# Performance work log

Hardware: AMD Instinct MI355X
Metric: run time of the kernel (lower is better)

Reference implementation:

```python
import jax, jax.numpy as jnp
import numpy as np

D_MODEL = 1024
NUM_HEADS = 16
HEAD_DIM = D_MODEL // NUM_HEADS


def setup_inputs() -> dict:
    key = jax.random.key(0)
    ks = jax.random.split(key, 11)
    B, S = 2, 2048
    s = 1.0 / np.sqrt(D_MODEL)
    return {
        "q": jax.random.normal(ks[0], (B, S, D_MODEL), jnp.float32),
        "k": jax.random.normal(ks[1], (B, S, D_MODEL), jnp.float32),
        "v": jax.random.normal(ks[2], (B, S, D_MODEL), jnp.float32),
        "Wq": jax.random.normal(ks[3], (D_MODEL, D_MODEL), jnp.float32) * s,
        "bq": jnp.zeros((D_MODEL,), jnp.float32),
        "Wk": jax.random.normal(ks[4], (D_MODEL, D_MODEL), jnp.float32) * s,
        "bk": jnp.zeros((D_MODEL,), jnp.float32),
        "Wv": jax.random.normal(ks[5], (D_MODEL, D_MODEL), jnp.float32) * s,
        "bv": jnp.zeros((D_MODEL,), jnp.float32),
        "Wo": jax.random.normal(ks[6], (D_MODEL, D_MODEL), jnp.float32) * s,
        "bo": jnp.zeros((D_MODEL,), jnp.float32),
    }


def _split_heads(x):
    B, S, _ = x.shape
    return x.reshape(B, S, NUM_HEADS, HEAD_DIM).transpose(0, 2, 1, 3)  # [B,H,S,Dh]


def reference(q, k, v, Wq, bq, Wk, bk, Wv, bv, Wo, bo):
    B, S, _ = q.shape
    qh = _split_heads(q @ Wq.T + bq)
    kh = _split_heads(k @ Wk.T + bk)
    vh = _split_heads(v @ Wv.T + bv)
    scale = 1.0 / jnp.sqrt(jnp.asarray(HEAD_DIM, qh.dtype))
    scores = jnp.einsum("bhqd,bhkd->bhqk", qh, kh) * scale  # [B,H,S,S]
    attn = jax.nn.softmax(scores, axis=-1)
    out = jnp.einsum("bhqk,bhkd->bhqd", attn, vh)
    out = out.transpose(0, 2, 1, 3).reshape(B, S, D_MODEL)
    return out @ Wo.T + bo
```

## Files before the change

kernel.cpp:

```cpp
#include <hip/hip_runtime.h>
#include <cstdint>
#include <cstddef>

#define DEVI __device__ __forceinline__

typedef short bf16x8 __attribute__((ext_vector_type(8)));
typedef short bf16x4 __attribute__((ext_vector_type(4)));
typedef float f32x4 __attribute__((ext_vector_type(4)));
typedef float f32x16 __attribute__((ext_vector_type(16)));
typedef unsigned short u16x4 __attribute__((ext_vector_type(4)));

constexpr int D_MODEL = 1024;
constexpr int HEADS = 16;
constexpr int DH = 64;
constexpr int SEQ = 2048;
constexpr int KDIM = 1024;

DEVI unsigned short f2bf(float f) {
  union { float f; unsigned u; } v; v.f = f;
  unsigned r = v.u + 0x7fffu + ((v.u >> 16) & 1u);
  return (unsigned short)(r >> 16);
}

DEVI unsigned pkbf(float a, float b) {
  return __builtin_amdgcn_perm(__float_as_uint(b), __float_as_uint(a), 0x07060302u);
}

DEVI void cp16(const void* g, void* l) {
  __builtin_amdgcn_global_load_lds(
      (const __attribute__((address_space(1))) void*)g,
      (__attribute__((address_space(3))) void*)l, 16, 0, 0);
}

DEVI f32x16 mfma_32x32x8(bf16x4 a, bf16x4 b, f32x16 c) {
#if __has_builtin(__builtin_amdgcn_mfma_f32_32x32x8bf16_1k)
  return __builtin_amdgcn_mfma_f32_32x32x8bf16_1k(a, b, c, 0, 0, 0);
#else
  asm volatile("v_mfma_f32_32x32x8_bf16 %0, %1, %2, %0" : "+v"(c) : "v"(a), "v"(b));
  return c;
#endif
}

#define BAR()        asm volatile("s_barrier" ::: "memory")
#define WAITVM(n)    asm volatile("s_waitcnt vmcnt(" #n ")" ::: "memory")

__global__ void __launch_bounds__(256) castall(
    const float* __restrict__ q, const float* __restrict__ k, const float* __restrict__ v,
    const float* __restrict__ Wq, const float* __restrict__ Wk,
    const float* __restrict__ Wv, const float* __restrict__ Wo,
    unsigned short* __restrict__ qb, unsigned short* __restrict__ kb, unsigned short* __restrict__ vb,
    unsigned short* __restrict__ Wqb, unsigned short* __restrict__ Wkb,
    unsigned short* __restrict__ Wvb, unsigned short* __restrict__ Wob) {
  int bid = blockIdx.x;
  const float* s; unsigned short* d; int off;
  if (bid < 12288) {
    int w = bid >> 12; off = bid & 4095;
    s = (w == 0) ? q : ((w == 1) ? k : v);
    d = (w == 0) ? qb : ((w == 1) ? kb : vb);
  } else {
    int w = (bid - 12288) >> 10; off = bid & 1023;
    s = (w == 0) ? Wq : ((w == 1) ? Wk : ((w == 2) ? Wv : Wo));
    d = (w == 0) ? Wqb : ((w == 1) ? Wkb : ((w == 2) ? Wvb : Wob));
  }
  int i = (off * 256 + threadIdx.x) * 4;
  float4 x = *(const float4*)(s + i);
  u16x4 o; o[0] = f2bf(x.x); o[1] = f2bf(x.y); o[2] = f2bf(x.z); o[3] = f2bf(x.w);
  *(u16x4*)(d + i) = o;
}

__global__ void __launch_bounds__(256) qkv_gemm(
    const unsigned short* __restrict__ qb, const unsigned short* __restrict__ kb,
    const unsigned short* __restrict__ vb,
    const unsigned short* __restrict__ Wqb, const unsigned short* __restrict__ Wkb,
    const unsigned short* __restrict__ Wvb,
    const float* __restrict__ bq, const float* __restrict__ bk, const float* __restrict__ bv,
    unsigned short* __restrict__ Qh, unsigned short* __restrict__ Kh,
    unsigned short* __restrict__ Vt, float qscale) {
  __shared__ unsigned short As[3][128 * 32];
  __shared__ unsigned short Bs[3][128 * 32];
  const int bid = blockIdx.x, seg = bid >> 8, inner = bid & 255;
  const int bm = inner & 31, bn = inner >> 5;
  const unsigned short* A = (seg == 0) ? qb : ((seg == 1) ? kb : vb);
  const unsigned short* W = (seg == 0) ? Wqb : ((seg == 1) ? Wkb : Wvb);
  const float* bias = (seg == 0) ? bq : ((seg == 1) ? bk : bv);
  unsigned short* O = (seg == 0) ? Qh : ((seg == 1) ? Kh : Vt);
  const float oscale = (seg == 0) ? qscale : 1.0f;
  const int mode = (seg == 2) ? 1 : 0;

  const int tid = threadIdx.x, lane = tid & 63, wave = tid >> 6;
  const int l16 = lane & 15, quad = lane >> 4;
  const int wm = (wave >> 1) * 64, wn = (wave & 1) * 64;
  const int sw = (l16 >> 1) & 3;
  f32x4 acc[4][4] = {};

  const int r0 = tid >> 2, p0 = tid & 3;
  const int c0 = (p0 ^ ((r0 >> 1) & 3)) * 8;
  const int r1 = (256 + tid) >> 2;
  const int c1 = (p0 ^ ((r1 >> 1) & 3)) * 8;
  const unsigned short* Arow0 = A + (size_t)(bm * 128 + r0) * KDIM + c0;
  const unsigned short* Arow1 = A + (size_t)(bm * 128 + r1) * KDIM + c1;
  const unsigned short* Wrow0 = W + (size_t)(bn * 128 + r0) * KDIM + c0;
  const unsigned short* Wrow1 = W + (size_t)(bn * 128 + r1) * KDIM + c1;

#define QKV_ISSUE(K0, P)                                    \
  do {                                                      \
    cp16(Arow0 + (K0), &As[P][tid * 8]);                    \
    cp16(Arow1 + (K0), &As[P][(256 + tid) * 8]);            \
    cp16(Wrow0 + (K0), &Bs[P][tid * 8]);                    \
    cp16(Wrow1 + (K0), &Bs[P][(256 + tid) * 8]);            \
  } while (0)

#define QKV_COMPUTE(P)                                                             \
  do {                                                                             \
    bf16x8 af[4], bfr[4];                                                          \
    _Pragma("unroll") for (int t = 0; t < 4; ++t)                                  \
        af[t] = *(const bf16x8*)&As[P][(wm + t * 16 + l16) * 32 + ((quad ^ sw) * 8)]; \
    _Pragma("unroll") for (int t = 0; t < 4; ++t)                                  \
        bfr[t] = *(const bf16x8*)&Bs[P][(wn + t * 16 + l16) * 32 + ((quad ^ sw) * 8)]; \
    _Pragma("unroll") for (int i = 0; i < 4; ++i)                                  \
        _Pragma("unroll") for (int j = 0; j < 4; ++j)                              \
            acc[i][j] = __builtin_amdgcn_mfma_f32_16x16x32_bf16(af[i], bfr[j],     \
                                                                acc[i][j], 0, 0, 0); \
  } while (0)

  QKV_ISSUE(0, 0);
  QKV_ISSUE(32, 1);
  for (int k = 0; k < 30; k += 3) {
    BAR(); QKV_ISSUE((k + 2) * 32, 2); WAITVM(8); BAR(); QKV_COMPUTE(0);
    BAR(); QKV_ISSUE((k + 3) * 32, 0); WAITVM(8); BAR(); QKV_COMPUTE(1);
    BAR(); QKV_ISSUE((k + 4) * 32, 1); WAITVM(8); BAR(); QKV_COMPUTE(2);
  }
  WAITVM(4); BAR(); QKV_COMPUTE(0);
  WAITVM(0); BAR(); QKV_COMPUTE(1);

#pragma unroll
  for (int i = 0; i < 4; ++i) {
#pragma unroll
    for (int j = 0; j < 4; ++j) {
      const int col = bn * 128 + wn + j * 16 + l16;
      const float bv = bias[col];
#pragma unroll
      for (int r = 0; r < 4; ++r) {
        const int row = bm * 128 + wm + i * 16 + quad * 4 + r;
        const float val = (acc[i][j][r] + bv) * oscale;
        const int b = row >> 11, s = row & (SEQ - 1);
        const int h = col >> 6, d = col & (DH - 1);
        size_t idx;
        if (mode == 0) idx = ((size_t)(b * HEADS + h) * SEQ + s) * DH + d;
        else           idx = ((size_t)(b * HEADS + h) * DH + d) * SEQ + s;
        O[idx] = f2bf(val);
      }
    }
  }
#undef QKV_ISSUE
#undef QKV_COMPUTE
}

__global__ void __launch_bounds__(256) out_gemm(const unsigned short* __restrict__ AO,
                                                const unsigned short* __restrict__ Wob,
                                                const float* __restrict__ bo,
                                                float* __restrict__ out) {
  __shared__ unsigned short As[3][64 * 32];
  __shared__ unsigned short Bs[3][128 * 32];
  const int bid = blockIdx.x, bm = bid & 63, bn = bid >> 6;
  const int tid = threadIdx.x, lane = tid & 63, wave = tid >> 6;
  const int l16 = lane & 15, quad = lane >> 4;
  const int wn = wave * 32;
  const int sw = (l16 >> 1) & 3;
  f32x4 acc[4][2] = {};

  const int ra = tid >> 2, pa = tid & 3;
  const int ca = (pa ^ ((ra >> 1) & 3)) * 8;
  const int r1 = (256 + tid) >> 2;
  const int c1 = (pa ^ ((r1 >> 1) & 3)) * 8;
  const unsigned short* Arow  = AO + (size_t)(bm * 64 + ra) * KDIM + ca;
  const unsigned short* Wrow0 = Wob + (size_t)(bn * 128 + ra) * KDIM + ca;
  const unsigned short* Wrow1 = Wob + (size_t)(bn * 128 + r1) * KDIM + c1;

#define OUT_ISSUE(K0, P)                                    \
  do {                                                      \
    cp16(Arow + (K0), &As[P][tid * 8]);                     \
    cp16(Wrow0 + (K0), &Bs[P][tid * 8]);                    \
    cp16(Wrow1 + (K0), &Bs[P][(256 + tid) * 8]);            \
  } while (0)

#define OUT_COMPUTE(P)                                                             \
  do {                                                                             \
    bf16x8 af[4], bfr[2];                                                          \
    _Pragma("unroll") for (int t = 0; t < 4; ++t)                                  \
        af[t] = *(const bf16x8*)&As[P][(t * 16 + l16) * 32 + ((quad ^ sw) * 8)];   \
    _Pragma("unroll") for (int u = 0; u < 2; ++u)                                  \
        bfr[u] = *(const bf16x8*)&Bs[P][(wn + u * 16 + l16) * 32 + ((quad ^ sw) * 8)]; \
    _Pragma("unroll") for (int i = 0; i < 4; ++i)                                  \
        _Pragma("unroll") for (int j = 0; j < 2; ++j)                              \
            acc[i][j] = __builtin_amdgcn_mfma_f32_16x16x32_bf16(af[i], bfr[j],     \
                                                                acc[i][j], 0, 0, 0); \
  } while (0)

  OUT_ISSUE(0, 0);
  OUT_ISSUE(32, 1);
  for (int k = 0; k < 30; k += 3) {
    BAR(); OUT_ISSUE((k + 2) * 32, 2); WAITVM(6); BAR(); OUT_COMPUTE(0);
    BAR(); OUT_ISSUE((k + 3) * 32, 0); WAITVM(6); BAR(); OUT_COMPUTE(1);
    BAR(); OUT_ISSUE((k + 4) * 32, 1); WAITVM(6); BAR(); OUT_COMPUTE(2);
  }
  WAITVM(3); BAR(); OUT_COMPUTE(0);
  WAITVM(0); BAR(); OUT_COMPUTE(1);

#pragma unroll
  for (int i = 0; i < 4; ++i)
#pragma unroll
    for (int j = 0; j < 2; ++j) {
      const int col = bn * 128 + wn + j * 16 + l16;
      const float bv = bo[col];
#pragma unroll
      for (int r = 0; r < 4; ++r) {
        const int row = bm * 64 + i * 16 + quad * 4 + r;
        out[(size_t)row * D_MODEL + col] = acc[i][j][r] + bv;
      }
    }
#undef OUT_ISSUE
#undef OUT_COMPUTE
}

__global__ void __launch_bounds__(256) attn(const unsigned short* __restrict__ Qh,
                                            const unsigned short* __restrict__ Kh,
                                            const unsigned short* __restrict__ Vt,
                                            unsigned short* __restrict__ AO) {
  __shared__ __align__(16) char smem[32768];
  unsigned short* Ks = (unsigned short*)smem;
  unsigned short* Vs = (unsigned short*)(smem + 16384);

  const int bid = blockIdx.x;
  const int qt = bid >> 5, head = bid & 31, b = head >> 4, h = head & 15;
  const int tid = threadIdx.x;
  const int lane = tid & 63, wave = tid >> 6;
  const int wq = wave >> 1, wk = wave & 1;
  const int l31 = lane & 31, hh = lane >> 5;

  const unsigned short* Qhead = Qh + (size_t)(b * HEADS + h) * SEQ * DH;
  const unsigned short* Khead = Kh + (size_t)(b * HEADS + h) * SEQ * DH;
  const unsigned short* Vhead = Vt + (size_t)(b * HEADS + h) * DH * SEQ;

  const int qrow = qt * 64 + wq * 32 + l31;
  bf16x8 aq[4];
#pragma unroll
  for (int it = 0; it < 4; ++it)
    aq[it] = *(const bf16x8*)&Qhead[(size_t)qrow * DH + it * 16 + hh * 8];

  f32x16 oacc[2] = {};
  float lsum = 0.f;

  for (int kc = 0; kc < SEQ / 128; ++kc) {
#pragma unroll
    for (int c = 0; c < 4; ++c) {
      int s = c * 256 + tid;
      int row = s >> 3, pblk = s & 7;
      int jb = pblk ^ (row & 7);
      cp16(Khead + (size_t)(kc * 128 + row) * DH + jb * 8, &Ks[s * 8]);
    }
#pragma unroll
    for (int c = 0; c < 4; ++c) {
      int s = c * 256 + tid;
      int d = s >> 4, pblk = s & 15;
      int jb = pblk ^ (d & 7);
      cp16(Vhead + (size_t)d * SEQ + kc * 128 + jb * 8, &Vs[s * 8]);
    }
    asm volatile("s_waitcnt vmcnt(0)" ::: "memory");
    __syncthreads();

#pragma unroll
    for (int sub = 0; sub < 2; ++sub) {
      const int kb32 = sub * 64 + wk * 32;
      const int key = kb32 + l31;

      f32x16 sa = {};
#pragma unroll
      for (int it = 0; it < 4; ++it) {
        const int sblk = (2 * it + hh) ^ (key & 7);
        bf16x8 ak = *(const bf16x8*)&Ks[key * 64 + sblk * 8];
        sa = __builtin_amdgcn_mfma_f32_32x32x16_bf16(ak, aq[it], sa, 0, 0, 0);
      }

      float p[16];
#pragma unroll
      for (int r = 0; r < 16; ++r) {
        p[r] = __builtin_amdgcn_exp2f(sa[r]);
        lsum += p[r];
      }
      bf16x4 pk[4];
#pragma unroll
      for (int g = 0; g < 4; ++g) {
        union { unsigned u[2]; bf16x4 s; } c;
        c.u[0] = pkbf(p[4 * g + 0], p[4 * g + 1]);
        c.u[1] = pkbf(p[4 * g + 2], p[4 * g + 3]);
        pk[g] = c.s;
      }

#pragma unroll
      for (int g = 0; g < 4; ++g) {
        const int gblk = sub * 8 + wk * 4 + g;
#pragma unroll
        for (int dh2 = 0; dh2 < 2; ++dh2) {
          const int d = dh2 * 32 + l31;
          const int sv = gblk ^ (d & 7);
          bf16x4 av = *(const bf16x4*)&Vs[d * 128 + sv * 8 + hh * 4];
          oacc[dh2] = mfma_32x32x8(av, pk[g], oacc[dh2]);
        }
      }
    }
    __syncthreads();
  }

  lsum += __shfl_xor(lsum, 32);

  float* epiF = (float*)smem;
  float* lbuf = (float*)(smem + 16384);
  unsigned short* Oq = (unsigned short*)(smem + 17408);

  if (l31 == lane) lbuf[wave * 32 + l31] = lsum;
  if (wk == 1) {
#pragma unroll
    for (int dh2 = 0; dh2 < 2; ++dh2)
#pragma unroll
      for (int r = 0; r < 16; ++r) {
        const int d = dh2 * 32 + (r & 3) + 8 * (r >> 2) + 4 * hh;
        epiF[wq * 2048 + d * 32 + l31] = oacc[dh2][r];
      }
  }
  __syncthreads();

  if (wk == 0) {
    const float linv = 1.0f / (lsum + lbuf[(wq * 2 + 1) * 32 + l31]);
#pragma unroll
    for (int dh2 = 0; dh2 < 2; ++dh2) {
#pragma unroll
      for (int r = 0; r < 16; r += 2) {
        const int d = dh2 * 32 + (r & 3) + 8 * (r >> 2) + 4 * hh;
        const float v0 = (oacc[dh2][r]     + epiF[wq * 2048 + d * 32 + l31]) * linv;
        const float v1 = (oacc[dh2][r + 1] + epiF[wq * 2048 + (d + 1) * 32 + l31]) * linv;
        *(unsigned*)&Oq[wq * 2176 + l31 * 68 + d] = pkbf(v0, v1);
      }
    }
  }
  __syncthreads();

  {
    const int qloc = tid >> 2, d0 = (tid & 3) * 16;
    const int base = (qloc >> 5) * 2176 + (qloc & 31) * 68 + d0;
    unsigned u[8];
#pragma unroll
    for (int i = 0; i < 8; ++i) u[i] = *(const unsigned*)&Oq[base + i * 2];
    unsigned short* dst = AO + ((size_t)(b * SEQ + qt * 64 + qloc)) * D_MODEL + h * 64 + d0;
    *(uint4*)dst       = make_uint4(u[0], u[1], u[2], u[3]);
    *(uint4*)(dst + 8) = make_uint4(u[4], u[5], u[6], u[7]);
  }
}

extern "C" void kernel_launch(void* const* d_in, const int* in_sizes, int n_in,
                              void* d_out, int out_size, void* d_ws, size_t ws_size,
                              hipStream_t stream) {
  const float* q  = (const float*)d_in[0];
  const float* k  = (const float*)d_in[1];
  const float* v  = (const float*)d_in[2];
  const float* Wq = (const float*)d_in[3];
  const float* bq = (const float*)d_in[4];
  const float* Wk = (const float*)d_in[5];
  const float* bk = (const float*)d_in[6];
  const float* Wv = (const float*)d_in[7];
  const float* bv = (const float*)d_in[8];
  const float* Wo = (const float*)d_in[9];
  const float* bo = (const float*)d_in[10];
  float* out = (float*)d_out;

  char* ws = (char*)d_ws;
  const size_t MB = 1ull << 20;
  unsigned short* qb  = (unsigned short*)(ws + 0 * MB);
  unsigned short* kb  = (unsigned short*)(ws + 8 * MB);
  unsigned short* vb  = (unsigned short*)(ws + 16 * MB);
  unsigned short* Wqb = (unsigned short*)(ws + 24 * MB);
  unsigned short* Wkb = (unsigned short*)(ws + 26 * MB);
  unsigned short* Wvb = (unsigned short*)(ws + 28 * MB);
  unsigned short* Wob = (unsigned short*)(ws + 30 * MB);
  unsigned short* Qh  = (unsigned short*)(ws + 32 * MB);
  unsigned short* Kh  = (unsigned short*)(ws + 40 * MB);
  unsigned short* Vt  = (unsigned short*)(ws + 48 * MB);
  unsigned short* AO  = (unsigned short*)(ws + 56 * MB);

  castall<<<16384, 256, 0, stream>>>(q, k, v, Wq, Wk, Wv, Wo,
                                     qb, kb, vb, Wqb, Wkb, Wvb, Wob);

  const float qscale = 0.125f * 1.44269504088896f;
  qkv_gemm<<<768, 256, 0, stream>>>(qb, kb, vb, Wqb, Wkb, Wvb, bq, bk, bv,
                                    Qh, Kh, Vt, qscale);

  attn<<<1024, 256, 0, stream>>>(Qh, Kh, Vt, AO);

  out_gemm<<<512, 256, 0, stream>>>(AO, Wob, bo, out);
}
```

Before: 235.2 us.

## Double-buffer K/V tiles in attention and switch PV to 32x32x16 MFMA

The attention kernel now keeps two LDS stages of K/V (64KB) and prefetches the next 128-key chunk while computing on the current one, replacing the load-wait-compute loop. The P·V product uses the 32x32x16 bf16 MFMA, with v_permlane32_swap rearranging the packed probabilities into the wider operand layout, which halves the number of PV MFMA instructions. It also raises wave priority around the compute section. The larger shared memory footprint may lower occupancy.

```diff
diff --git a/kernel.cpp b/kernel.cpp
--- a/kernel.cpp
+++ b/kernel.cpp
@@ -30,15 +30,6 @@
   __builtin_amdgcn_global_load_lds(
       (const __attribute__((address_space(1))) void*)g,
       (__attribute__((address_space(3))) void*)l, 16, 0, 0);
-}
-
-DEVI f32x16 mfma_32x32x8(bf16x4 a, bf16x4 b, f32x16 c) {
-#if __has_builtin(__builtin_amdgcn_mfma_f32_32x32x8bf16_1k)
-  return __builtin_amdgcn_mfma_f32_32x32x8bf16_1k(a, b, c, 0, 0, 0);
-#else
-  asm volatile("v_mfma_f32_32x32x8_bf16 %0, %1, %2, %0" : "+v"(c) : "v"(a), "v"(b));
-  return c;
-#endif
 }
 
 #define BAR()        asm volatile("s_barrier" ::: "memory")
@@ -227,9 +218,7 @@
                                             const unsigned short* __restrict__ Kh,
                                             const unsigned short* __restrict__ Vt,
                                             unsigned short* __restrict__ AO) {
-  __shared__ __align__(16) char smem[32768];
-  unsigned short* Ks = (unsigned short*)smem;
-  unsigned short* Vs = (unsigned short*)(smem + 16384);
+  __shared__ __align__(16) char smem[65536];
 
   const int bid = blockIdx.x;
   const int qt = bid >> 5, head = bid & 31, b = head >> 4, h = head & 15;
@@ -251,66 +240,81 @@
   f32x16 oacc[2] = {};
   float lsum = 0.f;
 
-  for (int kc = 0; kc < SEQ / 128; ++kc) {
-#pragma unroll
-    for (int c = 0; c < 4; ++c) {
-      int s = c * 256 + tid;
-      int row = s >> 3, pblk = s & 7;
-      int jb = pblk ^ (row & 7);
-      cp16(Khead + (size_t)(kc * 128 + row) * DH + jb * 8, &Ks[s * 8]);
-    }
-#pragma unroll
-    for (int c = 0; c < 4; ++c) {
-      int s = c * 256 + tid;
-      int d = s >> 4, pblk = s & 15;
-      int jb = pblk ^ (d & 7);
-      cp16(Vhead + (size_t)d * SEQ + kc * 128 + jb * 8, &Vs[s * 8]);
-    }
-    asm volatile("s_waitcnt vmcnt(0)" ::: "memory");
-    __syncthreads();
-
-#pragma unroll
-    for (int sub = 0; sub < 2; ++sub) {
-      const int kb32 = sub * 64 + wk * 32;
-      const int key = kb32 + l31;
-
-      f32x16 sa = {};
-#pragma unroll
-      for (int it = 0; it < 4; ++it) {
-        const int sblk = (2 * it + hh) ^ (key & 7);
-        bf16x8 ak = *(const bf16x8*)&Ks[key * 64 + sblk * 8];
-        sa = __builtin_amdgcn_mfma_f32_32x32x16_bf16(ak, aq[it], sa, 0, 0, 0);
-      }
-
-      float p[16];
-#pragma unroll
-      for (int r = 0; r < 16; ++r) {
-        p[r] = __builtin_amdgcn_exp2f(sa[r]);
-        lsum += p[r];
-      }
-      bf16x4 pk[4];
-#pragma unroll
-      for (int g = 0; g < 4; ++g) {
-        union { unsigned u[2]; bf16x4 s; } c;
-        c.u[0] = pkbf(p[4 * g + 0], p[4 * g + 1]);
-        c.u[1] = pkbf(p[4 * g + 2], p[4 * g + 3]);
-        pk[g] = c.s;
-      }
-
-#pragma unroll
-      for (int g = 0; g < 4; ++g) {
-        const int gblk = sub * 8 + wk * 4 + g;
-#pragma unroll
-        for (int dh2 = 0; dh2 < 2; ++dh2) {
-          const int d = dh2 * 32 + l31;
-          const int sv = gblk ^ (d & 7);
-          bf16x4 av = *(const bf16x4*)&Vs[d * 128 + sv * 8 + hh * 4];
-          oacc[dh2] = mfma_32x32x8(av, pk[g], oacc[dh2]);
-        }
-      }
-    }
-    __syncthreads();
-  }
+  const int krow = tid >> 3, kpb = tid & 7;
+  const int vd = tid >> 4, vpb = tid & 15;
+
+#define ATT_STAGE(KC, P)                                                      \
+  do {                                                                        \
+    unsigned short* Ksp = (unsigned short*)(smem + (P) * 32768);              \
+    unsigned short* Vsp = (unsigned short*)(smem + (P) * 32768 + 16384);      \
+    _Pragma("unroll") for (int c = 0; c < 4; ++c) {                           \
+      int row = c * 32 + krow;                                                \
+      int jb = kpb ^ (row & 7);                                               \
+      cp16(Khead + (size_t)((KC) * 128 + row) * DH + jb * 8,                  \
+           &Ksp[(c * 256 + tid) * 8]);                                        \
+    }                                                                         \
+    _Pragma("unroll") for (int c = 0; c < 4; ++c) {                           \
+      int d = c * 16 + vd;                                                    \
+      int jb = vpb ^ (d & 7);                                                 \
+      cp16(Vhead + (size_t)d * SEQ + (KC) * 128 + jb * 8,                     \
+           &Vsp[(c * 256 + tid) * 8]);                                        \
+    }                                                                         \
+  } while (0)
+
+#define ATT_COMPUTE(P)                                                        \
+  do {                                                                        \
+    const unsigned short* Ksp = (const unsigned short*)(smem + (P) * 32768);  \
+    const unsigned short* Vsp =                                               \
+        (const unsigned short*)(smem + (P) * 32768 + 16384);                  \
+    __builtin_amdgcn_s_setprio(1);                                            \
+    _Pragma("unroll") for (int sub = 0; sub < 2; ++sub) {                     \
+      const int kb32 = sub * 64 + wk * 32;                                    \
+      const int key = kb32 + l31;                                             \
+      f32x16 sa = {};                                                         \
+      _Pragma("unroll") for (int it = 0; it < 4; ++it) {                      \
+        const int sblk = (2 * it + hh) ^ (key & 7);                           \
+        bf16x8 ak = *(const bf16x8*)&Ksp[key * 64 + sblk * 8];                \
+        sa = __builtin_amdgcn_mfma_f32_32x32x16_bf16(ak, aq[it], sa, 0, 0, 0);\
+      }                                                                       \
+      float p[16];                                                            \
+      _Pragma("unroll") for (int r = 0; r < 16; ++r) {                        \
+        p[r] = __builtin_amdgcn_exp2f(sa[r]);                                 \
+        lsum += p[r];                                                         \
+      }                                                                       \
+      _Pragma("unroll") for (int c = 0; c < 2; ++c) {                         \
+        unsigned x0 = pkbf(p[8 * c + 0], p[8 * c + 1]);                       \
+        unsigned x1 = pkbf(p[8 * c + 2], p[8 * c + 3]);                       \
+        unsigned y0 = pkbf(p[8 * c + 4], p[8 * c + 5]);                       \
+        unsigned y1 = pkbf(p[8 * c + 6], p[8 * c + 7]);                       \
+        asm("v_permlane32_swap_b32 %0, %1" : "+v"(x0), "+v"(y0));             \
+        asm("v_permlane32_swap_b32 %0, %1" : "+v"(x1), "+v"(y1));             \
+        union { unsigned u[4]; bf16x8 s; } pb;                                \
+        pb.u[0] = x0; pb.u[1] = x1; pb.u[2] = y0; pb.u[3] = y1;               \
+        const int K8 = sub * 8 + wk * 4 + 2 * c + hh;                         \
+        _Pragma("unroll") for (int dh2 = 0; dh2 < 2; ++dh2) {                 \
+          const int d = dh2 * 32 + l31;                                       \
+          const int sv = K8 ^ (d & 7);                                        \
+          bf16x8 av = *(const bf16x8*)&Vsp[d * 128 + sv * 8];                 \
+          oacc[dh2] = __builtin_amdgcn_mfma_f32_32x32x16_bf16(av, pb.s,       \
+                                                              oacc[dh2],     \
+                                                              0, 0, 0);      \
+        }                                                                     \
+      }                                                                       \
+    }                                                                         \
+    __builtin_amdgcn_s_setprio(0);                                            \
+  } while (0)
+
+  ATT_STAGE(0, 0);
+  for (int kc = 0; kc < 15; ++kc) {
+    BAR();
+    ATT_STAGE(kc + 1, (kc + 1) & 1);
+    WAITVM(8);
+    BAR();
+    ATT_COMPUTE(kc & 1);
+  }
+  WAITVM(0);
+  BAR();
+  ATT_COMPUTE(1);
 
   lsum += __shfl_xor(lsum, 32);
 
@@ -355,6 +359,8 @@
     *(uint4*)dst       = make_uint4(u[0], u[1], u[2], u[3]);
     *(uint4*)(dst + 8) = make_uint4(u[4], u[5], u[6], u[7]);
   }
+#undef ATT_STAGE
+#undef ATT_COMPUTE
 }
 
 extern "C" void kernel_launch(void* const* d_in, const int* in_sizes, int n_in,
```

Measured after the change: 232.8 us. No clear change (-1.0%).
